# Kernel tuning notes

Hardware: AMD Instinct MI355X
Metric: run time of the kernel (lower is better)

The kernel has to match this reference:

```python
import jax, jax.numpy as jnp
import numpy as np


def setup_inputs() -> dict:
    key = jax.random.key(0)
    x = jax.random.normal(key, (32, 256, 128, 128), dtype=jnp.float32)
    return {"x": x}


def reference(x):
    b, c, h, w = x.shape
    # global average pool over spatial dims, per (b, c)
    pooled = jnp.mean(x, axis=(2, 3), keepdims=True)          # [b, c, 1, 1]
    # xn = (x * pooled).mean over channels -> [b, 1, h, w]
    xn = jnp.mean(x * pooled, axis=1, keepdims=True)
    # mean over batch -> [h, w]
    entro = jnp.mean(xn, axis=0)[0]
    e = entro.reshape(-1)
    emin = jnp.min(e)
    emax = jnp.max(e)
    e = (e - emin) / (emax - emin) * 255.0
    # torch.histc(bins=256, min=0, max=255): 256 uniform bins, last bin
    # right-inclusive -> matches jnp.histogram semantics.
    his, _ = jnp.histogram(e, bins=256, range=(0.0, 255.0))
    his = jax.lax.stop_gradient(his.astype(x.dtype)) / (h * w)
    entro_final = jnp.sum(his * -jnp.log(his + 1e-8))
    nz = jnp.count_nonzero(his).astype(x.dtype)
    entro_final = entro_final / nz
    s = jnp.mean(jax.nn.sigmoid(xn))
    return s + entro_final * 10.0
```

## Files before the change

### kernel.cpp

```cpp
#include <hip/hip_runtime.h>
#include <math.h>

#define BB 32
#define CC 256
#define HW 16384
#define BC (BB*CC)


__global__ __launch_bounds__(256) void pool_kernel(const float* __restrict__ x,
                                                   float* __restrict__ ws) {
    const int bc = blockIdx.x;
    const int t  = threadIdx.x;
    const float4* xv = (const float4*)x + (size_t)bc * (HW / 4);
    float s = 0.f;
#pragma unroll
    for (int i = 0; i < 16; ++i) {
        float4 v = xv[t + i * 256];
        s += v.x + v.y + v.z + v.w;
    }
    for (int o = 32; o > 0; o >>= 1) s += __shfl_down(s, o);
    __shared__ float part[4];
    if ((t & 63) == 0) part[t >> 6] = s;
    __syncthreads();
    if (t == 0) {
        float tot = part[0] + part[1] + part[2] + part[3];
        ws[bc] = tot * (1.0f / HW);
    }
    int tid = bc * 256 + t;
    if (tid < HW) ws[BC + tid] = 0.f;
    if (tid == 0) ws[BC + HW] = 0.f;
}

__global__ __launch_bounds__(256) void xn_kernel(const float* __restrict__ x,
                                                 float* __restrict__ ws) {
    const int b     = blockIdx.x >> 4;
    const int chunk = blockIdx.x & 15;
    const int t     = threadIdx.x;

    __shared__ float spool[CC];
    spool[t] = ws[b * CC + t];
    __syncthreads();

    const float4* xv = (const float4*)x;
    const size_t base = (size_t)b * CC * (HW / 4) + (size_t)chunk * 256 + t;

    float ax = 0.f, ay = 0.f, az = 0.f, aw = 0.f;
#pragma unroll 4
    for (int c = 0; c < CC; ++c) {
        float4 v = xv[base + (size_t)c * (HW / 4)];
        float p = spool[c];
        ax += v.x * p; ay += v.y * p; az += v.z * p; aw += v.w * p;
    }
    const float inv_c = 1.0f / CC;
    float xn0 = ax * inv_c, xn1 = ay * inv_c, xn2 = az * inv_c, xn3 = aw * inv_c;

    float* entro = ws + BC;
    const int hw = (chunk * 256 + t) * 4;
    const float inv_b = 1.0f / BB;
    atomicAdd(&entro[hw + 0], xn0 * inv_b);
    atomicAdd(&entro[hw + 1], xn1 * inv_b);
    atomicAdd(&entro[hw + 2], xn2 * inv_b);
    atomicAdd(&entro[hw + 3], xn3 * inv_b);

    float sg = 1.f / (1.f + expf(-xn0)) + 1.f / (1.f + expf(-xn1)) +
               1.f / (1.f + expf(-xn2)) + 1.f / (1.f + expf(-xn3));
    for (int o = 32; o > 0; o >>= 1) sg += __shfl_down(sg, o);
    __shared__ float part[4];
    if ((t & 63) == 0) part[t >> 6] = sg;
    __syncthreads();
    if (t == 0) {
        float tot = part[0] + part[1] + part[2] + part[3];
        atomicAdd(&ws[BC + HW], tot);
    }
}

__global__ __launch_bounds__(256) void finalize_kernel(const float* __restrict__ ws,
                                                       float* __restrict__ out) {
    const int t = threadIdx.x;
    const float* entro = ws + BC;

    float lmin = INFINITY, lmax = -INFINITY;
#pragma unroll
    for (int i = 0; i < 64; ++i) {
        float v = entro[t + i * 256];
        lmin = fminf(lmin, v);
        lmax = fmaxf(lmax, v);
    }
    for (int o = 32; o > 0; o >>= 1) {
        lmin = fminf(lmin, __shfl_down(lmin, o));
        lmax = fmaxf(lmax, __shfl_down(lmax, o));
    }
    __shared__ float smin[4], smax[4];
    __shared__ float bmin, bmax;
    if ((t & 63) == 0) { smin[t >> 6] = lmin; smax[t >> 6] = lmax; }
    __syncthreads();
    if (t == 0) {
        bmin = fminf(fminf(smin[0], smin[1]), fminf(smin[2], smin[3]));
        bmax = fmaxf(fmaxf(smax[0], smax[1]), fmaxf(smax[2], smax[3]));
    }
    __shared__ unsigned int hist[256];
    hist[t] = 0u;
    __syncthreads();

    const float emin = bmin, emax = bmax;
    const float scale = 256.0f / (emax - emin);
#pragma unroll
    for (int i = 0; i < 64; ++i) {
        float v = entro[t + i * 256];
        int idx = (int)floorf((v - emin) * scale);
        idx = idx < 0 ? 0 : (idx > 255 ? 255 : idx);
        atomicAdd(&hist[idx], 1u);
    }
    __syncthreads();

    const unsigned int h = hist[t];
    const float his = (float)h * (1.0f / HW);
    float term = (h > 0u) ? his * (-logf(his + 1e-8f)) : 0.f;
    float nzf  = (h > 0u) ? 1.f : 0.f;
    for (int o = 32; o > 0; o >>= 1) {
        term += __shfl_down(term, o);
        nzf  += __shfl_down(nzf, o);
    }
    __shared__ float sterm[4], snz[4];
    if ((t & 63) == 0) { sterm[t >> 6] = term; snz[t >> 6] = nzf; }
    __syncthreads();
    if (t == 0) {
        float ent = sterm[0] + sterm[1] + sterm[2] + sterm[3];
        float nz  = snz[0] + snz[1] + snz[2] + snz[3];
        float sig = ws[BC + HW] * (1.0f / ((float)BB * (float)HW));
        out[0] = sig + (ent / nz) * 10.0f;
    }
}

extern "C" void kernel_launch(void* const* d_in, const int* in_sizes, int n_in,
                              void* d_out, int out_size, void* d_ws, size_t ws_size,
                              hipStream_t stream) {
    const float* x = (const float*)d_in[0];
    float* out = (float*)d_out;
    float* ws  = (float*)d_ws;

    pool_kernel<<<BC, 256, 0, stream>>>(x, ws);
    xn_kernel<<<BB * 16, 256, 0, stream>>>(x, ws);
    finalize_kernel<<<1, 256, 0, stream>>>(ws, out);
}
```

Measured before the change: 765.0 us.

## Split channel reduction across blocks and replace atomics with a batch-reduce kernel

```diff
diff --git a/kernel.cpp b/kernel.cpp
--- a/kernel.cpp
+++ b/kernel.cpp
@@ -4,14 +4,18 @@
 #define BB 32
 #define CC 256
 #define HW 16384
+#define HW4 4096
 #define BC (BB*CC)
 
+#define XN_OFF    8192
+#define ENTRO_OFF (XN_OFF + 4*BB*HW)
+#define SIG_OFF   (ENTRO_OFF + HW)
 
 __global__ __launch_bounds__(256) void pool_kernel(const float* __restrict__ x,
                                                    float* __restrict__ ws) {
     const int bc = blockIdx.x;
     const int t  = threadIdx.x;
-    const float4* xv = (const float4*)x + (size_t)bc * (HW / 4);
+    const float4* xv = (const float4*)x + (size_t)bc * HW4;
     float s = 0.f;
 #pragma unroll
     for (int i = 0; i < 16; ++i) {
@@ -26,65 +30,84 @@
         float tot = part[0] + part[1] + part[2] + part[3];
         ws[bc] = tot * (1.0f / HW);
     }
-    int tid = bc * 256 + t;
-    if (tid < HW) ws[BC + tid] = 0.f;
-    if (tid == 0) ws[BC + HW] = 0.f;
+    if (bc == 0 && t == 0) ws[SIG_OFF] = 0.f;
 }
 
-__global__ __launch_bounds__(256) void xn_kernel(const float* __restrict__ x,
-                                                 float* __restrict__ ws) {
-    const int b     = blockIdx.x >> 4;
-    const int chunk = blockIdx.x & 15;
+__global__ __launch_bounds__(256) void xn_partial_kernel(const float* __restrict__ x,
+                                                         float* __restrict__ ws) {
+    const int bid   = blockIdx.x;
+    const int cg    = bid & 3;
+    const int chunk = (bid >> 2) & 15;
+    const int b     = bid >> 6;
     const int t     = threadIdx.x;
 
-    __shared__ float spool[CC];
-    spool[t] = ws[b * CC + t];
+    __shared__ float spool[64];
+    if (t < 64) spool[t] = ws[b * CC + cg * 64 + t];
     __syncthreads();
 
     const float4* xv = (const float4*)x;
-    const size_t base = (size_t)b * CC * (HW / 4) + (size_t)chunk * 256 + t;
+    const size_t base = (size_t)b * CC * HW4 + (size_t)(cg * 64) * HW4
+                      + (size_t)chunk * 256 + t;
 
     float ax = 0.f, ay = 0.f, az = 0.f, aw = 0.f;
-#pragma unroll 4
-    for (int c = 0; c < CC; ++c) {
-        float4 v = xv[base + (size_t)c * (HW / 4)];
+#pragma unroll 8
+    for (int c = 0; c < 64; ++c) {
+        float4 v = xv[base + (size_t)c * HW4];
         float p = spool[c];
         ax += v.x * p; ay += v.y * p; az += v.z * p; aw += v.w * p;
     }
+    float4 o; o.x = ax; o.y = ay; o.z = az; o.w = aw;
+    float4* xnp = (float4*)(ws + XN_OFF);
+    xnp[(size_t)(cg * BB + b) * HW4 + chunk * 256 + t] = o;
+}
+
+__global__ __launch_bounds__(256) void entro_sig_kernel(float* __restrict__ ws) {
+    const int j = blockIdx.x * 256 + threadIdx.x;
+    const int t = threadIdx.x;
+    const float4* xnp = (const float4*)(ws + XN_OFF);
     const float inv_c = 1.0f / CC;
-    float xn0 = ax * inv_c, xn1 = ay * inv_c, xn2 = az * inv_c, xn3 = aw * inv_c;
 
-    float* entro = ws + BC;
-    const int hw = (chunk * 256 + t) * 4;
+    float ex = 0.f, ey = 0.f, ez = 0.f, ew = 0.f;
+    float sg = 0.f;
+#pragma unroll 4
+    for (int b = 0; b < BB; ++b) {
+        float4 s0 = xnp[(size_t)(0 * BB + b) * HW4 + j];
+        float4 s1 = xnp[(size_t)(1 * BB + b) * HW4 + j];
+        float4 s2 = xnp[(size_t)(2 * BB + b) * HW4 + j];
+        float4 s3 = xnp[(size_t)(3 * BB + b) * HW4 + j];
+        float xnx = (s0.x + s1.x + s2.x + s3.x) * inv_c;
+        float xny = (s0.y + s1.y + s2.y + s3.y) * inv_c;
+        float xnz = (s0.z + s1.z + s2.z + s3.z) * inv_c;
+        float xnw = (s0.w + s1.w + s2.w + s3.w) * inv_c;
+        ex += xnx; ey += xny; ez += xnz; ew += xnw;
+        sg += 1.f / (1.f + expf(-xnx)) + 1.f / (1.f + expf(-xny)) +
+              1.f / (1.f + expf(-xnz)) + 1.f / (1.f + expf(-xnw));
+    }
     const float inv_b = 1.0f / BB;
-    atomicAdd(&entro[hw + 0], xn0 * inv_b);
-    atomicAdd(&entro[hw + 1], xn1 * inv_b);
-    atomicAdd(&entro[hw + 2], xn2 * inv_b);
-    atomicAdd(&entro[hw + 3], xn3 * inv_b);
+    float4 e; e.x = ex * inv_b; e.y = ey * inv_b; e.z = ez * inv_b; e.w = ew * inv_b;
+    ((float4*)(ws + ENTRO_OFF))[j] = e;
 
-    float sg = 1.f / (1.f + expf(-xn0)) + 1.f / (1.f + expf(-xn1)) +
-               1.f / (1.f + expf(-xn2)) + 1.f / (1.f + expf(-xn3));
     for (int o = 32; o > 0; o >>= 1) sg += __shfl_down(sg, o);
     __shared__ float part[4];
     if ((t & 63) == 0) part[t >> 6] = sg;
     __syncthreads();
     if (t == 0) {
         float tot = part[0] + part[1] + part[2] + part[3];
-        atomicAdd(&ws[BC + HW], tot);
+        atomicAdd(&ws[SIG_OFF], tot);
     }
 }
 
 __global__ __launch_bounds__(256) void finalize_kernel(const float* __restrict__ ws,
                                                        float* __restrict__ out) {
     const int t = threadIdx.x;
-    const float* entro = ws + BC;
+    const float4* ev = (const float4*)(ws + ENTRO_OFF);
 
     float lmin = INFINITY, lmax = -INFINITY;
 #pragma unroll
-    for (int i = 0; i < 64; ++i) {
-        float v = entro[t + i * 256];
-        lmin = fminf(lmin, v);
-        lmax = fmaxf(lmax, v);
+    for (int i = 0; i < 16; ++i) {
+        float4 v = ev[t + i * 256];
+        lmin = fminf(lmin, fminf(fminf(v.x, v.y), fminf(v.z, v.w)));
+        lmax = fmaxf(lmax, fmaxf(fmaxf(v.x, v.y), fmaxf(v.z, v.w)));
     }
     for (int o = 32; o > 0; o >>= 1) {
         lmin = fminf(lmin, __shfl_down(lmin, o));
@@ -105,11 +128,20 @@
     const float emin = bmin, emax = bmax;
     const float scale = 256.0f / (emax - emin);
 #pragma unroll
-    for (int i = 0; i < 64; ++i) {
-        float v = entro[t + i * 256];
-        int idx = (int)floorf((v - emin) * scale);
-        idx = idx < 0 ? 0 : (idx > 255 ? 255 : idx);
-        atomicAdd(&hist[idx], 1u);
+    for (int i = 0; i < 16; ++i) {
+        float4 v = ev[t + i * 256];
+        int i0 = (int)floorf((v.x - emin) * scale);
+        int i1 = (int)floorf((v.y - emin) * scale);
+        int i2 = (int)floorf((v.z - emin) * scale);
+        int i3 = (int)floorf((v.w - emin) * scale);
+        i0 = i0 < 0 ? 0 : (i0 > 255 ? 255 : i0);
+        i1 = i1 < 0 ? 0 : (i1 > 255 ? 255 : i1);
+        i2 = i2 < 0 ? 0 : (i2 > 255 ? 255 : i2);
+        i3 = i3 < 0 ? 0 : (i3 > 255 ? 255 : i3);
+        atomicAdd(&hist[i0], 1u);
+        atomicAdd(&hist[i1], 1u);
+        atomicAdd(&hist[i2], 1u);
+        atomicAdd(&hist[i3], 1u);
     }
     __syncthreads();
 
@@ -127,7 +159,7 @@
     if (t == 0) {
         float ent = sterm[0] + sterm[1] + sterm[2] + sterm[3];
         float nz  = snz[0] + snz[1] + snz[2] + snz[3];
-        float sig = ws[BC + HW] * (1.0f / ((float)BB * (float)HW));
+        float sig = ws[SIG_OFF] * (1.0f / ((float)BB * (float)HW));
         out[0] = sig + (ent / nz) * 10.0f;
     }
 }
@@ -140,6 +172,7 @@
     float* ws  = (float*)d_ws;
 
     pool_kernel<<<BC, 256, 0, stream>>>(x, ws);
-    xn_kernel<<<BB * 16, 256, 0, stream>>>(x, ws);
+    xn_partial_kernel<<<BB * 16 * 4, 256, 0, stream>>>(x, ws);
+    entro_sig_kernel<<<16, 256, 0, stream>>>(ws);
     finalize_kernel<<<1, 256, 0, stream>>>(ws, out);
 }
```

Measured after the change: 793.0 us. 3.7% more time.
